# Kernel optimization log

Measured on AMD Instinct MI355X. Metric: run time of the kernel, lower is better.

The kernel has to match this reference:

```python
import jax, jax.numpy as jnp
import numpy as np

DIM = 2048
NUM_EXPERTS = 8
N_TOKENS = 8192
SPARSITY = 0.8  # sparsity_constraint parameter (used only to derive static k)
K = max(1, int(SPARSITY * NUM_EXPERTS))  # = 6


def setup_inputs() -> dict:
    key = jax.random.key(0)
    ks = jax.random.split(key, 5)
    scale = 1.0 / np.sqrt(DIM)
    x = jax.random.normal(ks[0], (N_TOKENS, DIM), dtype=jnp.float32)
    Wg = jax.random.uniform(ks[1], (NUM_EXPERTS, DIM), jnp.float32, -scale, scale)
    bg = jax.random.uniform(ks[2], (NUM_EXPERTS,), jnp.float32, -scale, scale)
    We = jax.random.uniform(ks[3], (NUM_EXPERTS, DIM, DIM), jnp.float32, -scale, scale)
    be = jax.random.uniform(ks[4], (NUM_EXPERTS, DIM), jnp.float32, -scale, scale)
    return {"x": x, "Wg": Wg, "bg": bg, "We": We, "be": be}


def reference(x, Wg, bg, We, be):
    # gate scores: [N, E]
    gate_scores = x @ Wg.T + bg
    # top-k expert indices per token: [N, K]
    _, topk_idx = jax.lax.top_k(gate_scores, K)
    # mask[n, e] = expert e is among token n's top-k: [N, E]
    mask = jnp.any(topk_idx[:, :, None] == jnp.arange(NUM_EXPERTS)[None, None, :], axis=1)
    # all expert outputs: [N, E, D]  (We is [E, out, in]; Linear = x @ W.T + b)
    expert_out = jnp.einsum('nd,efd->nef', x, We) + be[None, :, :]
    # combine: unweighted sum of selected experts' outputs (no gate weighting in source)
    out = jnp.sum(expert_out * mask[:, :, None].astype(x.dtype), axis=1)
    return out
```

## Files before the change

### kernel.cpp

```cpp
#include <hip/hip_runtime.h>
#include <hip/hip_bf16.h>
#include <stdint.h>

#define DIM 2048
#define NEXP 8
#define NTOK 8192
#define KSEL 6
#define NPAIR 28
#define SLOTS 92

typedef short bf16x8 __attribute__((ext_vector_type(8)));
typedef unsigned short u16x8 __attribute__((ext_vector_type(8)));
typedef float f32x4 __attribute__((ext_vector_type(4)));
typedef const __attribute__((address_space(1))) unsigned int GU32;
typedef __attribute__((address_space(3))) unsigned int LU32;

static constexpr int PA[NPAIR] = {0,0,0,0,0,0,0,1,1,1,1,1,1,2,2,2,2,2,3,3,3,3,4,4,4,5,5,6};
static constexpr int PB[NPAIR] = {1,2,3,4,5,6,7,2,3,4,5,6,7,3,4,5,6,7,4,5,6,7,5,6,7,6,7,7};

__device__ __forceinline__ unsigned short f2b(float f) {
  union { float f; uint32_t u; } v; v.f = f;
  return (unsigned short)((v.u + 0x7fffu + ((v.u >> 16) & 1u)) >> 16);
}

__global__ __launch_bounds__(256) void gatepair_kernel(
    const float* __restrict__ x, const float* __restrict__ Wg,
    const float* __restrict__ bg, const float* __restrict__ We,
    unsigned short* __restrict__ xB, int* __restrict__ pid,
    unsigned short* __restrict__ Wp, int fbase, int frows, int pairwBlocks) {
  int bid = blockIdx.x;
  int t = threadIdx.x;
  if (bid < pairwBlocks) {
    size_t pos = ((size_t)bid * 256 + t) * 8;
    size_t src = (size_t)fbase * DIM + pos;
    float v[NEXP][8];
    float s[8];
#pragma unroll
    for (int i = 0; i < 8; ++i) s[i] = 0.f;
#pragma unroll
    for (int e = 0; e < NEXP; ++e) {
      float4 v0 = *(const float4*)(We + (size_t)e * DIM * DIM + src);
      float4 v1 = *(const float4*)(We + (size_t)e * DIM * DIM + src + 4);
      v[e][0] = v0.x; v[e][1] = v0.y; v[e][2] = v0.z; v[e][3] = v0.w;
      v[e][4] = v1.x; v[e][5] = v1.y; v[e][6] = v1.z; v[e][7] = v1.w;
#pragma unroll
      for (int i = 0; i < 8; ++i) s[i] += v[e][i];
    }
    size_t chunk = (size_t)frows * DIM;
#pragma unroll
    for (int pp = 0; pp < NPAIR; ++pp) {
      int a = PA[pp], b = PB[pp];
      u16x8 o;
#pragma unroll
      for (int i = 0; i < 8; ++i) o[i] = f2b(s[i] - v[a][i] - v[b][i]);
      *(u16x8*)(Wp + (size_t)pp * chunk + pos) = o;
    }
    return;
  }
  int w = t >> 6, l = t & 63;
  int n = (bid - pairwBlocks) * 4 + w;
  const float* xr = x + (size_t)n * DIM;
  float xv[32];
#pragma unroll
  for (int j = 0; j < 8; ++j) {
    float4 v = *(const float4*)(xr + 4 * l + 256 * j);
    xv[4 * j + 0] = v.x; xv[4 * j + 1] = v.y;
    xv[4 * j + 2] = v.z; xv[4 * j + 3] = v.w;
  }
  unsigned short* xbr = xB + (size_t)n * DIM;
#pragma unroll
  for (int j = 0; j < 8; ++j) {
    ushort4 o;
    o.x = f2b(xv[4 * j + 0]); o.y = f2b(xv[4 * j + 1]);
    o.z = f2b(xv[4 * j + 2]); o.w = f2b(xv[4 * j + 3]);
    *(ushort4*)(xbr + 4 * l + 256 * j) = o;
  }
  float sc[NEXP];
#pragma unroll
  for (int e = 0; e < NEXP; ++e) {
    const float* wr = Wg + e * DIM;
    float s = 0.f;
#pragma unroll
    for (int j = 0; j < 8; ++j) {
      float4 v = *(const float4*)(wr + 4 * l + 256 * j);
      s += xv[4 * j + 0] * v.x + xv[4 * j + 1] * v.y +
           xv[4 * j + 2] * v.z + xv[4 * j + 3] * v.w;
    }
#pragma unroll
    for (int off = 32; off > 0; off >>= 1) s += __shfl_xor(s, off, 64);
    sc[e] = s + bg[e];
  }
  if (l == 0) {
    int ex0 = -1, ex1 = -1;
#pragma unroll
    for (int e = 0; e < NEXP; ++e) {
      int rank = 0;
#pragma unroll
      for (int j = 0; j < NEXP; ++j)
        rank += (sc[j] > sc[e]) || (sc[j] == sc[e] && j < e);
      if (rank >= KSEL) { if (ex0 < 0) ex0 = e; else if (ex1 < 0) ex1 = e; }
    }
    pid[n] = ex0 * (15 - ex0) / 2 + (ex1 - ex0 - 1);
  }
}

__global__ __launch_bounds__(256) void pairw_kernel(
    const float* __restrict__ We, unsigned short* __restrict__ Wp,
    int fbase, int frows) {
  size_t pos = ((size_t)blockIdx.x * 256 + threadIdx.x) * 8;
  size_t src = (size_t)fbase * DIM + pos;
  float v[NEXP][8];
  float s[8];
#pragma unroll
  for (int i = 0; i < 8; ++i) s[i] = 0.f;
#pragma unroll
  for (int e = 0; e < NEXP; ++e) {
    float4 v0 = *(const float4*)(We + (size_t)e * DIM * DIM + src);
    float4 v1 = *(const float4*)(We + (size_t)e * DIM * DIM + src + 4);
    v[e][0] = v0.x; v[e][1] = v0.y; v[e][2] = v0.z; v[e][3] = v0.w;
    v[e][4] = v1.x; v[e][5] = v1.y; v[e][6] = v1.z; v[e][7] = v1.w;
#pragma unroll
    for (int i = 0; i < 8; ++i) s[i] += v[e][i];
  }
  size_t chunk = (size_t)frows * DIM;
#pragma unroll
  for (int pp = 0; pp < NPAIR; ++pp) {
    int a = PA[pp], b = PB[pp];
    u16x8 o;
#pragma unroll
    for (int i = 0; i < 8; ++i) o[i] = f2b(s[i] - v[a][i] - v[b][i]);
    *(u16x8*)(Wp + (size_t)pp * chunk + pos) = o;
  }
}

__global__ __launch_bounds__(1024) void bucket_kernel(
    const int* __restrict__ pid, const float* __restrict__ be,
    int* __restrict__ cnt, int* __restrict__ meta,
    int* __restrict__ slotP, int* __restrict__ slotM0,
    int* __restrict__ list, float* __restrict__ biasPair) {
  int t = threadIdx.x;
  if (blockIdx.x == 1) {
#pragma unroll
    for (int it = 0; it < 2; ++it) {
      int f = t + 1024 * it;
      float v[NEXP]; float s = 0.f;
#pragma unroll
      for (int e = 0; e < NEXP; ++e) { v[e] = be[e * DIM + f]; s += v[e]; }
#pragma unroll
      for (int pp = 0; pp < NPAIR; ++pp)
        biasPair[pp * DIM + f] = s - v[PA[pp]] - v[PB[pp]];
    }
    return;
  }
  __shared__ int lcnt[NPAIR];
  __shared__ int lpos[NPAIR];
  if (t < NPAIR) { lcnt[t] = 0; lpos[t] = 0; }
  __syncthreads();
  int p[8];
#pragma unroll
  for (int j = 0; j < 8; ++j) {
    p[j] = pid[t + 1024 * j];
    atomicAdd(&lcnt[p[j]], 1);
  }
  __syncthreads();
  if (t == 0) {
    int ts = 0;
    for (int q = 0; q < NPAIR; ++q) {
      cnt[q] = lcnt[q];
      for (int s0 = 0; s0 < lcnt[q]; s0 += 128) {
        slotP[ts] = q; slotM0[ts] = s0; ++ts;
      }
    }
    meta[0] = ts;
  }
  __syncthreads();
#pragma unroll
  for (int j = 0; j < 8; ++j) {
    int pos = atomicAdd(&lpos[p[j]], 1);
    list[p[j] * NTOK + pos] = t + 1024 * j;
  }
}

__global__ __launch_bounds__(512, 4) void gemm_pair(
    const unsigned short* __restrict__ A, const unsigned short* __restrict__ Wp,
    const int* __restrict__ cnt, const int* __restrict__ list,
    const int* __restrict__ meta, const int* __restrict__ slotP,
    const int* __restrict__ slotM0, const float* __restrict__ biasPair,
    float* __restrict__ out, int fbase, int frows) {
  __shared__ unsigned short sA[128 * 64];
  __shared__ unsigned short sB[256 * 64];
  __shared__ int sRows[128];
  int total = meta[0];
  if (blockIdx.y >= total) return;
  int slot = total - 1 - blockIdx.y;
  int ft = blockIdx.x;
  int p = slotP[slot];
  int m0 = slotM0[slot];
  int c = cnt[p];

  int t = threadIdx.x;
  int w = t >> 6, l = t & 63;
  int wm = w >> 2, wn = w & 3;
  int quad = l >> 4, lr = l & 15;
  int cs = (l & 7) ^ ((l >> 3) & 7);
  bool live = (wm == 0) || (m0 + 64 < c);

  if (t < 128) {
    int idx = m0 + t;
    if (idx >= c) idx = c - 1;
    sRows[t] = list[p * NTOK + idx];
  }
  __syncthreads();

  size_t rowOffA[2], rowOffB[4];
#pragma unroll
  for (int i = 0; i < 2; ++i)
    rowOffA[i] = (size_t)sRows[i * 64 + w * 8 + (l >> 3)] * DIM;
  const unsigned short* Bb =
      Wp + (size_t)p * frows * DIM + (size_t)ft * 256 * DIM;
#pragma unroll
  for (int i = 0; i < 4; ++i)
    rowOffB[i] = (size_t)(i * 64 + w * 8 + (l >> 3)) * DIM;

  f32x4 acc[4][4];
#pragma unroll
  for (int mi = 0; mi < 4; ++mi)
#pragma unroll
    for (int ni = 0; ni < 4; ++ni) {
      acc[mi][ni][0] = 0.f; acc[mi][ni][1] = 0.f;
      acc[mi][ni][2] = 0.f; acc[mi][ni][3] = 0.f;
    }

  for (int k0 = 0; k0 < DIM; k0 += 64) {
#pragma unroll
    for (int i = 0; i < 2; ++i)
      __builtin_amdgcn_global_load_lds((GU32*)(A + rowOffA[i] + k0 + cs * 8),
          (LU32*)(sA + (i * 64 + w * 8) * 64), 16, 0, 0);
#pragma unroll
    for (int i = 0; i < 4; ++i)
      __builtin_amdgcn_global_load_lds((GU32*)(Bb + rowOffB[i] + k0 + cs * 8),
          (LU32*)(sB + (i * 64 + w * 8) * 64), 16, 0, 0);
    __syncthreads();
    if (live) {
#pragma unroll
      for (int ks = 0; ks < 2; ++ks) {
        bf16x8 aF[4], bF[4];
#pragma unroll
        for (int mi = 0; mi < 4; ++mi)
          aF[mi] = *(const bf16x8*)(sA + (wm * 64 + mi * 16 + lr) * 64 +
                                    (((ks << 2) | quad) ^ (lr & 7)) * 8);
#pragma unroll
        for (int ni = 0; ni < 4; ++ni)
          bF[ni] = *(const bf16x8*)(sB + (wn * 64 + ni * 16 + lr) * 64 +
                                    (((ks << 2) | quad) ^ (lr & 7)) * 8);
#pragma unroll
        for (int mi = 0; mi < 4; ++mi)
#pragma unroll
          for (int ni = 0; ni < 4; ++ni)
            acc[mi][ni] = __builtin_amdgcn_mfma_f32_16x16x32_bf16(aF[mi], bF[ni], acc[mi][ni], 0, 0, 0);
      }
    }
    __syncthreads();
  }

  if (!live) return;
  int f0 = fbase + ft * 256;
  float bb[4];
#pragma unroll
  for (int ni = 0; ni < 4; ++ni)
    bb[ni] = biasPair[p * DIM + f0 + wn * 64 + ni * 16 + lr];
#pragma unroll
  for (int mi = 0; mi < 4; ++mi) {
#pragma unroll
    for (int i = 0; i < 4; ++i) {
      int lrow = wm * 64 + mi * 16 + quad * 4 + i;
      if (m0 + lrow < c) {
        float* orow = out + (size_t)sRows[lrow] * DIM + f0;
#pragma unroll
        for (int ni = 0; ni < 4; ++ni)
          orow[wn * 64 + ni * 16 + lr] = acc[mi][ni][i] + bb[ni];
      }
    }
  }
}

extern "C" void kernel_launch(void* const* d_in, const int* in_sizes, int n_in,
                              void* d_out, int out_size, void* d_ws, size_t ws_size,
                              hipStream_t stream) {
  const float* x  = (const float*)d_in[0];
  const float* Wg = (const float*)d_in[1];
  const float* bg = (const float*)d_in[2];
  const float* We = (const float*)d_in[3];
  const float* be = (const float*)d_in[4];
  float* out = (float*)d_out;

  char* ws = (char*)d_ws;
  unsigned short* xB = (unsigned short*)ws; ws += (size_t)NTOK * DIM * 2;
  int* pid = (int*)ws;          ws += (size_t)NTOK * 4;
  int* cnt = (int*)ws;          ws += 128;
  int* meta = (int*)ws;         ws += 128;
  int* slotP = (int*)ws;        ws += 512;
  int* slotM0 = (int*)ws;       ws += 512;
  int* list = (int*)ws;         ws += (size_t)NPAIR * NTOK * 4;
  float* biasPair = (float*)ws; ws += (size_t)NPAIR * DIM * 4;
  unsigned short* Wp = (unsigned short*)ws;

  size_t avail = ws_size - (size_t)(ws - (char*)d_ws);
  int NR = 1;
  while (NR < 8 && (size_t)NPAIR * DIM * (size_t)(DIM / NR) * 2 > avail) NR <<= 1;
  int frows = DIM / NR;

  int pairwBlocks = (frows * DIM) / 2048;
  gatepair_kernel<<<pairwBlocks + NTOK / 4, 256, 0, stream>>>(
      x, Wg, bg, We, xB, pid, Wp, 0, frows, pairwBlocks);
  bucket_kernel<<<2, 1024, 0, stream>>>(pid, be, cnt, meta, slotP, slotM0,
                                        list, biasPair);
  gemm_pair<<<dim3(frows / 256, SLOTS), 512, 0, stream>>>(
      xB, Wp, cnt, list, meta, slotP, slotM0, biasPair, out, 0, frows);
  for (int r = 1; r < NR; ++r) {
    int fbase = r * frows;
    pairw_kernel<<<(frows * DIM) / 2048, 256, 0, stream>>>(We, Wp, fbase, frows);
    gemm_pair<<<dim3(frows / 256, SLOTS), 512, 0, stream>>>(
        xB, Wp, cnt, list, meta, slotP, slotM0, biasPair, out, fbase, frows);
  }
}
```

Before: 456.8 us.

## Double-buffer LDS tiles in pair GEMM to overlap global loads with MFMA

Splits the shared A and B tiles into two buffers and software-pipelines the K loop: the next tile is loaded directly into LDS while MFMAs run on the current one, using partial vmcnt waits instead of full syncthreads. It also raises wave priority around the MFMA block and lowers launch-bounds occupancy to 2 blocks per CU because the doubled LDS needs more space. The aim is to hide global-load latency. The costs are fewer resident blocks and one redundant final load of the last tile to keep the wait count uniform.

```diff
diff --git a/kernel.cpp b/kernel.cpp
--- a/kernel.cpp
+++ b/kernel.cpp
@@ -181,14 +181,16 @@
   }
 }
 
-__global__ __launch_bounds__(512, 4) void gemm_pair(
+__global__ __launch_bounds__(512, 2) void gemm_pair(
     const unsigned short* __restrict__ A, const unsigned short* __restrict__ Wp,
     const int* __restrict__ cnt, const int* __restrict__ list,
     const int* __restrict__ meta, const int* __restrict__ slotP,
     const int* __restrict__ slotM0, const float* __restrict__ biasPair,
     float* __restrict__ out, int fbase, int frows) {
-  __shared__ unsigned short sA[128 * 64];
-  __shared__ unsigned short sB[256 * 64];
+  __shared__ unsigned short sA0[128 * 64];
+  __shared__ unsigned short sA1[128 * 64];
+  __shared__ unsigned short sB0[256 * 64];
+  __shared__ unsigned short sB1[256 * 64];
   __shared__ int sRows[128];
   int total = meta[0];
   if (blockIdx.y >= total) return;
@@ -231,37 +233,60 @@
       acc[mi][ni][2] = 0.f; acc[mi][ni][3] = 0.f;
     }
 
-  for (int k0 = 0; k0 < DIM; k0 += 64) {
-#pragma unroll
-    for (int i = 0; i < 2; ++i)
-      __builtin_amdgcn_global_load_lds((GU32*)(A + rowOffA[i] + k0 + cs * 8),
-          (LU32*)(sA + (i * 64 + w * 8) * 64), 16, 0, 0);
-#pragma unroll
-    for (int i = 0; i < 4; ++i)
-      __builtin_amdgcn_global_load_lds((GU32*)(Bb + rowOffB[i] + k0 + cs * 8),
-          (LU32*)(sB + (i * 64 + w * 8) * 64), 16, 0, 0);
-    __syncthreads();
-    if (live) {
-#pragma unroll
-      for (int ks = 0; ks < 2; ++ks) {
-        bf16x8 aF[4], bF[4];
-#pragma unroll
-        for (int mi = 0; mi < 4; ++mi)
-          aF[mi] = *(const bf16x8*)(sA + (wm * 64 + mi * 16 + lr) * 64 +
-                                    (((ks << 2) | quad) ^ (lr & 7)) * 8);
-#pragma unroll
-        for (int ni = 0; ni < 4; ++ni)
-          bF[ni] = *(const bf16x8*)(sB + (wn * 64 + ni * 16 + lr) * 64 +
-                                    (((ks << 2) | quad) ^ (lr & 7)) * 8);
-#pragma unroll
-        for (int mi = 0; mi < 4; ++mi)
-#pragma unroll
-          for (int ni = 0; ni < 4; ++ni)
-            acc[mi][ni] = __builtin_amdgcn_mfma_f32_16x16x32_bf16(aF[mi], bF[ni], acc[mi][ni], 0, 0, 0);
-      }
-    }
-    __syncthreads();
-  }
+#define STAGE(SAd, SBd, kk) do {                                              \
+    _Pragma("unroll")                                                         \
+    for (int i = 0; i < 2; ++i)                                               \
+      __builtin_amdgcn_global_load_lds((GU32*)(A + rowOffA[i] + (kk) + cs * 8),\
+          (LU32*)((SAd) + (i * 64 + w * 8) * 64), 16, 0, 0);                  \
+    _Pragma("unroll")                                                         \
+    for (int i = 0; i < 4; ++i)                                               \
+      __builtin_amdgcn_global_load_lds((GU32*)(Bb + rowOffB[i] + (kk) + cs * 8),\
+          (LU32*)((SBd) + (i * 64 + w * 8) * 64), 16, 0, 0);                  \
+  } while (0)
+
+#define COMPUTE(SAs, SBs) do {                                                \
+    if (live) {                                                               \
+      _Pragma("unroll")                                                       \
+      for (int ks = 0; ks < 2; ++ks) {                                        \
+        bf16x8 aF[4], bF[4];                                                  \
+        _Pragma("unroll")                                                     \
+        for (int mi = 0; mi < 4; ++mi)                                        \
+          aF[mi] = *(const bf16x8*)((SAs) + (wm * 64 + mi * 16 + lr) * 64 +   \
+                                    (((ks << 2) | quad) ^ (lr & 7)) * 8);     \
+        _Pragma("unroll")                                                     \
+        for (int ni = 0; ni < 4; ++ni)                                        \
+          bF[ni] = *(const bf16x8*)((SBs) + (wn * 64 + ni * 16 + lr) * 64 +   \
+                                    (((ks << 2) | quad) ^ (lr & 7)) * 8);     \
+        __builtin_amdgcn_s_setprio(1);                                        \
+        _Pragma("unroll")                                                     \
+        for (int mi = 0; mi < 4; ++mi)                                        \
+          _Pragma("unroll")                                                   \
+          for (int ni = 0; ni < 4; ++ni)                                      \
+            acc[mi][ni] = __builtin_amdgcn_mfma_f32_16x16x32_bf16(            \
+                aF[mi], bF[ni], acc[mi][ni], 0, 0, 0);                        \
+        __builtin_amdgcn_s_setprio(0);                                        \
+      }                                                                       \
+    }                                                                         \
+  } while (0)
+
+  STAGE(sA0, sB0, 0);
+#pragma unroll 1
+  for (int tt = 0; tt < 16; ++tt) {
+    int k0 = tt * 128;
+    STAGE(sA1, sB1, k0 + 64);
+    asm volatile("s_waitcnt vmcnt(6)" ::: "memory");
+    __builtin_amdgcn_s_barrier();
+    COMPUTE(sA0, sB0);
+    __builtin_amdgcn_s_barrier();
+    int kn = (tt < 15) ? k0 + 128 : k0 + 64;
+    STAGE(sA0, sB0, kn);
+    asm volatile("s_waitcnt vmcnt(6)" ::: "memory");
+    __builtin_amdgcn_s_barrier();
+    COMPUTE(sA1, sB1);
+    __builtin_amdgcn_s_barrier();
+  }
+#undef STAGE
+#undef COMPUTE
 
   if (!live) return;
   int f0 = fbase + ft * 256;
```

Result: slower. 471.7 us (+3.3%).
